# Kernel optimization log

Measured on AMD Instinct MI355X. Metric: run time of the kernel, lower is better.

## Reference

```python
import jax, jax.numpy as jnp
import numpy as np

L, I, D, N, K = 2, 8192, 2048, 2048, 32


def setup_inputs() -> dict:
    key = jax.random.key(0)
    k1, k2, k3, k4 = jax.random.split(key, 4)
    gate = jax.random.normal(k1, (L, I, D), dtype=jnp.float32) * (1.0 / np.sqrt(D).astype(np.float32))
    up = jax.random.normal(k2, (L, I, D), dtype=jnp.float32) * (1.0 / np.sqrt(D).astype(np.float32))
    down = jax.random.normal(k3, (L, D, I), dtype=jnp.float32) * (1.0 / np.sqrt(I).astype(np.float32))
    x = jax.random.normal(k4, (N, D), dtype=jnp.float32)
    return {"x": x, "gate": gate, "up": up, "down": down, "layer_idx": 0, "top_k": K}


def reference(x, gate, up, down, layer_idx, top_k):
    # Select frozen per-layer MLP weights
    g_w = gate[layer_idx]   # [I, D]
    u_w = up[layer_idx]     # [I, D]
    d_w = down[layer_idx]   # [D, I]
    # Full gate activations (needed to pick top-k neurons)
    g_full = jax.nn.silu(x @ g_w.T)                    # [N, I]
    # Top-k neurons per token by |gate activation|
    _, idx = jax.lax.top_k(jnp.abs(g_full), top_k)     # [N, K] int32
    g_sel = jnp.take_along_axis(g_full, idx, axis=-1)  # [N, K]
    # Gather-dot up projection: only the selected neuron rows
    u_sel = jnp.einsum('nkd,nd->nk', u_w[idx], x)      # [N, K]
    gu = g_sel * u_sel                                 # [N, K]
    # Gather-weighted-sum down projection: down.T rows for selected neurons
    out = jnp.einsum('nk,nkd->nd', gu, jnp.swapaxes(d_w, 0, 1)[idx])  # [N, D]
    return out
```

## Files before the change

kernel.cpp:

```cpp
#include <hip/hip_runtime.h>
#include <hip/hip_fp16.h>
#include <math.h>

constexpr int LI = 8192;
constexpr int LD = 2048;
constexpr int LN = 2048;
constexpr int LK = 32;
constexpr int CAP = 192;
constexpr int DEPTH = 96;

typedef short short8 __attribute__((ext_vector_type(8)));
typedef unsigned short ushort8 __attribute__((ext_vector_type(8)));
typedef _Float16 half8 __attribute__((ext_vector_type(8)));
typedef float f32x4 __attribute__((ext_vector_type(4)));
typedef const __attribute__((address_space(1))) void* gas1_t;
typedef __attribute__((address_space(3))) void* las3_t;

__device__ __forceinline__ void gload16(const void* g, void* l) {
    __builtin_amdgcn_global_load_lds((gas1_t)g, (las3_t)l, 16, 0, 0);
}
__device__ __forceinline__ unsigned short f2bf_rne(float f) {
    unsigned u = __float_as_uint(f);
    return (unsigned short)((u + 0x7fffu + ((u >> 16) & 1u)) >> 16);
}
__device__ __forceinline__ unsigned short f2h_rne(float f) {
    return __half_as_ushort(__float2half(f));
}
__device__ __forceinline__ float h2f(unsigned short u) {
    return __half2float(__ushort_as_half(u));
}

__global__ __launch_bounds__(256) void k_cvt2(
    const float* __restrict__ x, const float* __restrict__ gate,
    const int* __restrict__ layer_idx,
    unsigned short* __restrict__ xh, unsigned short* __restrict__ wh,
    int* __restrict__ ghist)
{
    if (blockIdx.x >= 2560) {
        int t = threadIdx.x;
        #pragma unroll
        for (int b = 0; b < 32; ++b) ghist[t * 32 + b] = 0;
        return;
    }
    const float* src; unsigned short* dst; int n8, bid, nb;
    if (blockIdx.x < 512) {
        src = x; dst = xh; n8 = (LN * LD) / 8; bid = blockIdx.x; nb = 512;
    } else {
        src = gate + (size_t)layer_idx[0] * LI * LD; dst = wh;
        n8 = (LI * LD) / 8; bid = blockIdx.x - 512; nb = 2048;
    }
    int i = bid * 256 + threadIdx.x;
    int stride = nb * 256;
    for (; i < n8; i += stride) {
        f32x4 v0 = *(const f32x4*)(src + 8 * (size_t)i);
        f32x4 v1 = *(const f32x4*)(src + 8 * (size_t)i + 4);
        ushort8 h;
        h[0] = f2h_rne(v0[0]); h[1] = f2h_rne(v0[1]);
        h[2] = f2h_rne(v0[2]); h[3] = f2h_rne(v0[3]);
        h[4] = f2h_rne(v1[0]); h[5] = f2h_rne(v1[1]);
        h[6] = f2h_rne(v1[2]); h[7] = f2h_rne(v1[3]);
        ((ushort8*)dst)[i] = h;
    }
}

__global__ __launch_bounds__(256) void k_gemmT(
    const unsigned short* __restrict__ xh, const unsigned short* __restrict__ wh,
    const float* __restrict__ down, const int* __restrict__ layer_idx,
    unsigned short* __restrict__ zk, unsigned short* __restrict__ dTb)
{
    __shared__ char smem[32768];
    const int tid = threadIdx.x;

    if (blockIdx.x >= 1024) {
        float (*t)[65] = (float(*)[65])smem;
        const float* __restrict__ dw = down + (size_t)layer_idx[0] * LD * LI;
        const int bid2 = blockIdx.x - 1024;
        const int bi = (bid2 & 127) * 64;
        const int bd = (bid2 >> 7) * 64;
        const int tx = tid & 63, ty = tid >> 6;
        #pragma unroll
        for (int it = 0; it < 16; ++it) {
            int r = ty + it * 4;
            t[r][tx] = dw[(size_t)(bd + r) * LI + bi + tx];
        }
        __syncthreads();
        #pragma unroll
        for (int it = 0; it < 16; ++it) {
            int rr = ty + it * 4;
            dTb[(size_t)(bi + rr) * LD + bd + tx] = f2bf_rne(t[tx][rr]);
        }
        return;
    }

    short* Ah = (short*)smem;
    short* Bh = (short*)smem + 8192;

    const int w = tid >> 6, lane = tid & 63;
    const int flat = blockIdx.x;
    const int xcd  = flat & 7;
    const int l    = flat >> 3;
    const int bi = (xcd * 8 + (l & 7)) * 128;
    const int bn = (l >> 3) * 128;

    const int srow   = w * 32 + (lane >> 3);
    const int schunk = (lane & 7) ^ ((lane >> 3) & 7);
    const unsigned short* xbh = xh + (size_t)(bn + srow) * LD + schunk * 8;
    const unsigned short* wbh = wh + (size_t)(bi + srow) * LD + schunk * 8;

    f32x4 acc[4][4];
    #pragma unroll
    for (int m = 0; m < 4; ++m)
        #pragma unroll
        for (int n = 0; n < 4; ++n) acc[m][n] = (f32x4){0.f, 0.f, 0.f, 0.f};

    const int wm = (w >> 1) * 64, wn = (w & 1) * 64;

    #define STAGE(k0)                                                          \
        {                                                                      \
            _Pragma("unroll")                                                  \
            for (int t = 0; t < 4; ++t) {                                      \
                int ldo = (w * 32 + t * 8) * 64;                               \
                size_t go = (size_t)t * 8 * LD + (k0);                         \
                gload16(xbh + go, Ah + ldo);                                   \
                gload16(wbh + go, Bh + ldo);                                   \
            }                                                                  \
        }

    STAGE(0);
    __syncthreads();
    for (int k0 = 0;;) {
        #pragma unroll
        for (int ks = 0; ks < 2; ++ks) {
            half8 a_h[4], b_h[4];
            #pragma unroll
            for (int m = 0; m < 4; ++m) {
                int lr = wm + m * 16 + (lane & 15);
                int lc = ks * 4 + (lane >> 4);
                a_h[m] = *(const half8*)(Ah + lr * 64 + ((lc ^ (lr & 7)) << 3));
            }
            #pragma unroll
            for (int n = 0; n < 4; ++n) {
                int lr = wn + n * 16 + (lane & 15);
                int lc = ks * 4 + (lane >> 4);
                b_h[n] = *(const half8*)(Bh + lr * 64 + ((lc ^ (lr & 7)) << 3));
            }
            #pragma unroll
            for (int m = 0; m < 4; ++m)
                #pragma unroll
                for (int n = 0; n < 4; ++n)
                    acc[m][n] = __builtin_amdgcn_mfma_f32_16x16x32_f16(a_h[m], b_h[n], acc[m][n], 0, 0, 0);
        }
        k0 += 64;
        if (k0 >= LD) break;
        __syncthreads();
        STAGE(k0);
        __syncthreads();
    }

    #pragma unroll
    for (int m = 0; m < 4; ++m) {
        int rb = bn + wm + m * 16 + (lane >> 4) * 4;
        #pragma unroll
        for (int n = 0; n < 4; ++n) {
            int cb = bi + wn + n * 16 + (lane & 15);
            #pragma unroll
            for (int r = 0; r < 4; ++r) {
                float zv = acc[m][n][r];
                float g = zv / (1.f + expf(-zv));
                zk[(size_t)(rb + r) * LI + cb] = f2h_rne(fabsf(g));
            }
        }
    }
    #undef STAGE
}

__global__ __launch_bounds__(256) void k_select(
    const unsigned short* __restrict__ zk, int* __restrict__ band,
    int* __restrict__ bandcnt, int* __restrict__ ghist, int* __restrict__ inv)
{
    __shared__ int hist[2048];
    __shared__ int sums[256];
    __shared__ int base_s;
    __shared__ int thrbin_s;

    const int row = blockIdx.x;
    const int tid = threadIdx.x;
    const int lane = tid & 63;
    const unsigned short* __restrict__ z = zk + (size_t)row * LI;

    if (tid == 0) { thrbin_s = 0; base_s = 0; }
    for (int i = tid; i < 2048; i += 256) hist[i] = 0;
    __syncthreads();

    ushort8 kv[4];
    #pragma unroll
    for (int c = 0; c < 4; ++c) {
        kv[c] = *(const ushort8*)(z + c * 2048 + tid * 8);
        #pragma unroll
        for (int j = 0; j < 8; ++j) {
            int b = (int)(kv[c][j] >> 2) - 3328;
            if (b > 0) {
                b = b > 2047 ? 2047 : b;
                atomicAdd(&hist[b], 1);
            }
        }
    }
    __syncthreads();

    int own = 0;
    #pragma unroll
    for (int b = 0; b < 8; ++b) own += hist[tid * 8 + b];
    sums[tid] = own;
    __syncthreads();
    for (int st = 1; st < 256; st <<= 1) {
        int v = (tid + st < 256) ? sums[tid + st] : 0;
        __syncthreads();
        sums[tid] += v;
        __syncthreads();
    }
    int after = (tid < 255) ? sums[tid + 1] : 0;
    if (after < LK && after + own >= LK) {
        int cum = after;
        for (int b = 7; b >= 0; --b) {
            cum += hist[tid * 8 + b];
            if (cum >= LK) { thrbin_s = tid * 8 + b; break; }
        }
    }
    __syncthreads();
    const float bandlo =
        h2f((unsigned short)((thrbin_s + 3328) << 2)) - 0.012f;

    #pragma unroll
    for (int c = 0; c < 4; ++c) {
        unsigned flags = 0;
        #pragma unroll
        for (int j = 0; j < 8; ++j) {
            if (h2f(kv[c][j]) >= bandlo) flags |= (1u << j);
        }
        int cnt = __popc(flags);
        int pre = cnt;
        #pragma unroll
        for (int o = 1; o < 64; o <<= 1) {
            int v = __shfl_up(pre, o);
            if (lane >= o) pre += v;
        }
        int wtotal = __shfl(pre, 63);
        int excl = pre - cnt;
        int wbase = 0;
        if (lane == 63 && wtotal) wbase = atomicAdd(&base_s, wtotal);
        wbase = __shfl(wbase, 63);
        int pos = wbase + excl;
        while (flags) {
            int j = __ffs(flags) - 1;
            flags &= flags - 1;
            if (pos < CAP) {
                int gi = c * 2048 + tid * 8 + j;
                band[row * CAP + pos] = gi;
                int p = atomicAdd(&ghist[gi], 1);
                if (p < DEPTH) inv[gi * DEPTH + p] = (row << 8) | pos;
            }
            ++pos;
        }
    }
    __syncthreads();
    if (tid == 0) bandcnt[row] = base_s < CAP ? base_s : CAP;
}

__global__ __launch_bounds__(256) void k_pair(
    const float* __restrict__ x, const float* __restrict__ gate,
    const float* __restrict__ up, const int* __restrict__ layer_idx,
    const int* __restrict__ ghist, const int* __restrict__ inv,
    float* __restrict__ gdot, float* __restrict__ udot)
{
    __shared__ float gs[LD];
    __shared__ float us[LD];
    const int j = blockIdx.x;
    const int tid = threadIdx.x;
    const int lane = tid & 63, w = tid >> 6;
    int nj = ghist[j];
    if (nj == 0) return;
    if (nj > DEPTH) nj = DEPTH;
    const float* __restrict__ gr = gate + (size_t)layer_idx[0] * LI * LD + (size_t)j * LD;
    const float* __restrict__ ur = up   + (size_t)layer_idx[0] * LI * LD + (size_t)j * LD;
    for (int i = tid * 4; i < LD; i += 1024) {
        *(f32x4*)&gs[i] = *(const f32x4*)(gr + i);
        *(f32x4*)&us[i] = *(const f32x4*)(ur + i);
    }
    __syncthreads();
    const int base = j * DEPTH;
    for (int e = w; e < nj; e += 4) {
        int packed = inv[base + e];
        int row = packed >> 8, slot = packed & 255;
        const float* __restrict__ xr = x + (size_t)row * LD;
        float gd0 = 0.f, gd1 = 0.f, ud0 = 0.f, ud1 = 0.f;
        #pragma unroll
        for (int it = 0; it < 8; it += 2) {
            int i0 = lane * 4 + it * 256;
            int i1 = i0 + 256;
            f32x4 xa = *(const f32x4*)(xr + i0);
            f32x4 xb = *(const f32x4*)(xr + i1);
            gd0 = fmaf(xa[0], gs[i0+0], gd0); gd0 = fmaf(xa[1], gs[i0+1], gd0);
            gd0 = fmaf(xa[2], gs[i0+2], gd0); gd0 = fmaf(xa[3], gs[i0+3], gd0);
            ud0 = fmaf(xa[0], us[i0+0], ud0); ud0 = fmaf(xa[1], us[i0+1], ud0);
            ud0 = fmaf(xa[2], us[i0+2], ud0); ud0 = fmaf(xa[3], us[i0+3], ud0);
            gd1 = fmaf(xb[0], gs[i1+0], gd1); gd1 = fmaf(xb[1], gs[i1+1], gd1);
            gd1 = fmaf(xb[2], gs[i1+2], gd1); gd1 = fmaf(xb[3], gs[i1+3], gd1);
            ud1 = fmaf(xb[0], us[i1+0], ud1); ud1 = fmaf(xb[1], us[i1+1], ud1);
            ud1 = fmaf(xb[2], us[i1+2], ud1); ud1 = fmaf(xb[3], us[i1+3], ud1);
        }
        float gd = gd0 + gd1, ud = ud0 + ud1;
        #pragma unroll
        for (int o = 32; o; o >>= 1) {
            gd += __shfl_down(gd, o);
            ud += __shfl_down(ud, o);
        }
        if (lane == 0) {
            gdot[(size_t)row * CAP + slot] = gd;
            udot[(size_t)row * CAP + slot] = ud;
        }
    }
}

__global__ __launch_bounds__(256) void k_finaldown(
    const int* __restrict__ band, const int* __restrict__ bandcnt,
    const float* __restrict__ gdot, const float* __restrict__ udot,
    const unsigned short* __restrict__ dTb, float* __restrict__ out)
{
    __shared__ float ckey[CAP];
    __shared__ float cgu[CAP];
    __shared__ int   cidx[CAP];
    __shared__ int   js[LK];
    __shared__ float wgt[LK];
    const int row = blockIdx.x;
    const int tid = threadIdx.x;
    const int lane = tid & 63;
    const int cnt = bandcnt[row];
    if (tid < CAP) { ckey[tid] = -1.f; cgu[tid] = 0.f; cidx[tid] = 0x7fffffff; }
    __syncthreads();
    if (tid < cnt) {
        float gd = gdot[(size_t)row * CAP + tid];
        float g = gd / (1.f + expf(-gd));
        ckey[tid] = fabsf(g);
        cgu[tid]  = g * udot[(size_t)row * CAP + tid];
        cidx[tid] = band[row * CAP + tid];
    }
    __syncthreads();
    if (tid < 64) {
        float k1 = ckey[lane], k2 = ckey[lane + 64], k3 = ckey[lane + 128];
        int   i1 = cidx[lane], i2 = cidx[lane + 64], i3 = cidx[lane + 128];
        int   p1 = lane, p2 = lane + 64, p3 = lane + 128;
        for (int slot = 0; slot < LK; ++slot) {
            float bk = k1; int bi_ = i1, bp = p1;
            if (k2 > bk || (k2 == bk && i2 < bi_)) { bk = k2; bi_ = i2; bp = p2; }
            if (k3 > bk || (k3 == bk && i3 < bi_)) { bk = k3; bi_ = i3; bp = p3; }
            #pragma unroll
            for (int o = 1; o < 64; o <<= 1) {
                float ok = __shfl_xor(bk, o);
                int  oi = __shfl_xor(bi_, o);
                int  op = __shfl_xor(bp, o);
                if (ok > bk || (ok == bk && oi < bi_)) { bk = ok; bi_ = oi; bp = op; }
            }
            if (lane == 0) {
                js[slot]  = bi_ & (LI - 1);
                wgt[slot] = cgu[bp < CAP ? bp : 0];
            }
            if (p1 == bp) { k1 = -1.f; i1 = 0x7fffffff; }
            if (p2 == bp) { k2 = -1.f; i2 = 0x7fffffff; }
            if (p3 == bp) { k3 = -1.f; i3 = 0x7fffffff; }
        }
    }
    __syncthreads();

    float a[8] = {0.f,0.f,0.f,0.f,0.f,0.f,0.f,0.f};
    #pragma unroll 4
    for (int k = 0; k < LK; ++k) {
        const ushort8 v = *(const ushort8*)(dTb + (size_t)js[k] * LD + tid * 8);
        float wv = wgt[k];
        #pragma unroll
        for (int e = 0; e < 8; ++e)
            a[e] = fmaf(wv, __uint_as_float(((unsigned)v[e]) << 16), a[e]);
    }
    float* o = out + (size_t)row * LD + tid * 8;
    f32x4 o0 = {a[0], a[1], a[2], a[3]};
    f32x4 o1 = {a[4], a[5], a[6], a[7]};
    *(f32x4*)o = o0;
    *(f32x4*)(o + 4) = o1;
}

extern "C" void kernel_launch(void* const* d_in, const int* in_sizes, int n_in,
                              void* d_out, int out_size, void* d_ws, size_t ws_size,
                              hipStream_t stream)
{
    const float* x      = (const float*)d_in[0];
    const float* gate   = (const float*)d_in[1];
    const float* up     = (const float*)d_in[2];
    const float* down   = (const float*)d_in[3];
    const int* layer_idx = (const int*)d_in[4];
    float* out = (float*)d_out;

    const size_t NC_ = (size_t)LN * CAP;
    char* p = (char*)d_ws;
    int*   band    = (int*)p;            p += NC_ * 4;
    int*   bandcnt = (int*)p;            p += (size_t)LN * 4;
    int*   ghist   = (int*)p;            p += (size_t)LI * 4;
    int*   inv     = (int*)p;            p += (size_t)LI * DEPTH * 4;
    float* gdot    = (float*)p;          p += NC_ * 4;
    float* udot    = (float*)p;          p += NC_ * 4;
    p = (char*)(((size_t)p + 255) & ~(size_t)255);

    const size_t xcnt = (size_t)LN * LD;
    const size_t wcnt = (size_t)LI * LD;
    unsigned short* xh = (unsigned short*)p;
    unsigned short* wh = xh + xcnt;
    unsigned short* zk = wh + wcnt;
    unsigned short* dTb = zk + (size_t)LN * LI;
    char* big_end = (char*)(dTb + (size_t)LI * LD);

    if ((size_t)(big_end - (char*)d_ws) > ws_size) return;

    k_cvt2<<<2561, 256, 0, stream>>>(x, gate, layer_idx, xh, wh, ghist);
    k_gemmT<<<5120, 256, 0, stream>>>(xh, wh, down, layer_idx, zk, dTb);
    k_select<<<LN, 256, 0, stream>>>(zk, band, bandcnt, ghist, inv);
    k_pair<<<LI, 256, 0, stream>>>(x, gate, up, layer_idx, ghist, inv, gdot, udot);
    k_finaldown<<<LN, 256, 0, stream>>>(band, bandcnt, gdot, udot, dTb, out);
}
```

Measured before the change: 270.5 us.

## Skip exact gate recompute for candidates clearly above the top-k threshold

The GEMM now stores the signed fp16 SiLU gate value, and selection splits candidates into sure-in ones and boundary ones using a second, higher threshold. Only boundary candidates get the exact fp32 gate dot product in k_pair. Sure candidates reuse the fp16 gate and compute the up dot from fp16 x. Gate rows are loaded only for neurons that have boundary entries. This cuts fp32 gate row traffic and FMA work, but the output now uses fp16-approximated gate and x values for most selected neurons, which lowers accuracy.

Result: faster. 244.9 us (-9.5%).

```diff
diff --git a/kernel.cpp b/kernel.cpp
--- a/kernel.cpp
+++ b/kernel.cpp
@@ -34,12 +34,15 @@
     const float* __restrict__ x, const float* __restrict__ gate,
     const int* __restrict__ layer_idx,
     unsigned short* __restrict__ xh, unsigned short* __restrict__ wh,
-    int* __restrict__ ghist)
+    int* __restrict__ ghist, int* __restrict__ gbnd)
 {
     if (blockIdx.x >= 2560) {
         int t = threadIdx.x;
         #pragma unroll
-        for (int b = 0; b < 32; ++b) ghist[t * 32 + b] = 0;
+        for (int b = 0; b < 32; ++b) {
+            ghist[t * 32 + b] = 0;
+            gbnd[t * 32 + b]  = 0;
+        }
         return;
     }
     const float* src; unsigned short* dst; int n8, bid, nb;
@@ -167,7 +170,7 @@
             for (int r = 0; r < 4; ++r) {
                 float zv = acc[m][n][r];
                 float g = zv / (1.f + expf(-zv));
-                zk[(size_t)(rb + r) * LI + cb] = f2h_rne(fabsf(g));
+                zk[(size_t)(rb + r) * LI + cb] = f2h_rne(g);
             }
         }
     }
@@ -176,7 +179,8 @@
 
 __global__ __launch_bounds__(256) void k_select(
     const unsigned short* __restrict__ zk, int* __restrict__ band,
-    int* __restrict__ bandcnt, int* __restrict__ ghist, int* __restrict__ inv)
+    int* __restrict__ bandcnt, int* __restrict__ ghist,
+    int* __restrict__ gbnd, int* __restrict__ inv)
 {
     __shared__ int hist[2048];
     __shared__ int sums[256];
@@ -198,7 +202,8 @@
         kv[c] = *(const ushort8*)(z + c * 2048 + tid * 8);
         #pragma unroll
         for (int j = 0; j < 8; ++j) {
-            int b = (int)(kv[c][j] >> 2) - 3328;
+            int ka = (int)(kv[c][j] & 0x7FFF);
+            int b = (ka >> 2) - 3328;
             if (b > 0) {
                 b = b > 2047 ? 2047 : b;
                 atomicAdd(&hist[b], 1);
@@ -229,13 +234,19 @@
     __syncthreads();
     const float bandlo =
         h2f((unsigned short)((thrbin_s + 3328) << 2)) - 0.012f;
+    const float thr_sure =
+        h2f((unsigned short)((thrbin_s + 1 + 3328) << 2)) + 0.024f;
 
     #pragma unroll
     for (int c = 0; c < 4; ++c) {
-        unsigned flags = 0;
+        unsigned flags = 0, bflags = 0;
         #pragma unroll
         for (int j = 0; j < 8; ++j) {
-            if (h2f(kv[c][j]) >= bandlo) flags |= (1u << j);
+            float kf = h2f((unsigned short)(kv[c][j] & 0x7FFF));
+            if (kf >= bandlo) {
+                flags |= (1u << j);
+                if (kf < thr_sure) bflags |= (1u << j);
+            }
         }
         int cnt = __popc(flags);
         int pre = cnt;
@@ -253,11 +264,13 @@
         while (flags) {
             int j = __ffs(flags) - 1;
             flags &= flags - 1;
+            int bnd = (bflags >> j) & 1;
             if (pos < CAP) {
                 int gi = c * 2048 + tid * 8 + j;
-                band[row * CAP + pos] = gi;
+                band[row * CAP + pos] = gi | (bnd << 15);
                 int p = atomicAdd(&ghist[gi], 1);
-                if (p < DEPTH) inv[gi * DEPTH + p] = (row << 8) | pos;
+                if (p < DEPTH) inv[gi * DEPTH + p] = (row << 9) | (bnd << 8) | pos;
+                if (bnd) atomicAdd(&gbnd[gi], 1);
             }
             ++pos;
         }
@@ -267,9 +280,11 @@
 }
 
 __global__ __launch_bounds__(256) void k_pair(
-    const float* __restrict__ x, const float* __restrict__ gate,
-    const float* __restrict__ up, const int* __restrict__ layer_idx,
-    const int* __restrict__ ghist, const int* __restrict__ inv,
+    const float* __restrict__ x, const unsigned short* __restrict__ xh,
+    const float* __restrict__ gate, const float* __restrict__ up,
+    const int* __restrict__ layer_idx,
+    const int* __restrict__ ghist, const int* __restrict__ gbnd,
+    const int* __restrict__ inv,
     float* __restrict__ gdot, float* __restrict__ udot)
 {
     __shared__ float gs[LD];
@@ -280,43 +295,68 @@
     int nj = ghist[j];
     if (nj == 0) return;
     if (nj > DEPTH) nj = DEPTH;
-    const float* __restrict__ gr = gate + (size_t)layer_idx[0] * LI * LD + (size_t)j * LD;
-    const float* __restrict__ ur = up   + (size_t)layer_idx[0] * LI * LD + (size_t)j * LD;
-    for (int i = tid * 4; i < LD; i += 1024) {
-        *(f32x4*)&gs[i] = *(const f32x4*)(gr + i);
+    const int hasb = gbnd[j];
+    const float* __restrict__ ur = up + (size_t)layer_idx[0] * LI * LD + (size_t)j * LD;
+    for (int i = tid * 4; i < LD; i += 1024)
         *(f32x4*)&us[i] = *(const f32x4*)(ur + i);
+    if (hasb) {
+        const float* __restrict__ gr = gate + (size_t)layer_idx[0] * LI * LD + (size_t)j * LD;
+        for (int i = tid * 4; i < LD; i += 1024)
+            *(f32x4*)&gs[i] = *(const f32x4*)(gr + i);
     }
     __syncthreads();
     const int base = j * DEPTH;
     for (int e = w; e < nj; e += 4) {
         int packed = inv[base + e];
-        int row = packed >> 8, slot = packed & 255;
-        const float* __restrict__ xr = x + (size_t)row * LD;
-        float gd0 = 0.f, gd1 = 0.f, ud0 = 0.f, ud1 = 0.f;
-        #pragma unroll
-        for (int it = 0; it < 8; it += 2) {
-            int i0 = lane * 4 + it * 256;
-            int i1 = i0 + 256;
-            f32x4 xa = *(const f32x4*)(xr + i0);
-            f32x4 xb = *(const f32x4*)(xr + i1);
-            gd0 = fmaf(xa[0], gs[i0+0], gd0); gd0 = fmaf(xa[1], gs[i0+1], gd0);
-            gd0 = fmaf(xa[2], gs[i0+2], gd0); gd0 = fmaf(xa[3], gs[i0+3], gd0);
-            ud0 = fmaf(xa[0], us[i0+0], ud0); ud0 = fmaf(xa[1], us[i0+1], ud0);
-            ud0 = fmaf(xa[2], us[i0+2], ud0); ud0 = fmaf(xa[3], us[i0+3], ud0);
-            gd1 = fmaf(xb[0], gs[i1+0], gd1); gd1 = fmaf(xb[1], gs[i1+1], gd1);
-            gd1 = fmaf(xb[2], gs[i1+2], gd1); gd1 = fmaf(xb[3], gs[i1+3], gd1);
-            ud1 = fmaf(xb[0], us[i1+0], ud1); ud1 = fmaf(xb[1], us[i1+1], ud1);
-            ud1 = fmaf(xb[2], us[i1+2], ud1); ud1 = fmaf(xb[3], us[i1+3], ud1);
-        }
-        float gd = gd0 + gd1, ud = ud0 + ud1;
-        #pragma unroll
-        for (int o = 32; o; o >>= 1) {
-            gd += __shfl_down(gd, o);
-            ud += __shfl_down(ud, o);
-        }
-        if (lane == 0) {
-            gdot[(size_t)row * CAP + slot] = gd;
-            udot[(size_t)row * CAP + slot] = ud;
+        int row = packed >> 9, bnd = (packed >> 8) & 1, slot = packed & 255;
+        if (bnd) {
+            const float* __restrict__ xr = x + (size_t)row * LD;
+            float gd0 = 0.f, gd1 = 0.f, ud0 = 0.f, ud1 = 0.f;
+            #pragma unroll
+            for (int it = 0; it < 8; it += 2) {
+                int i0 = lane * 4 + it * 256;
+                int i1 = i0 + 256;
+                f32x4 xa = *(const f32x4*)(xr + i0);
+                f32x4 xb = *(const f32x4*)(xr + i1);
+                gd0 = fmaf(xa[0], gs[i0+0], gd0); gd0 = fmaf(xa[1], gs[i0+1], gd0);
+                gd0 = fmaf(xa[2], gs[i0+2], gd0); gd0 = fmaf(xa[3], gs[i0+3], gd0);
+                ud0 = fmaf(xa[0], us[i0+0], ud0); ud0 = fmaf(xa[1], us[i0+1], ud0);
+                ud0 = fmaf(xa[2], us[i0+2], ud0); ud0 = fmaf(xa[3], us[i0+3], ud0);
+                gd1 = fmaf(xb[0], gs[i1+0], gd1); gd1 = fmaf(xb[1], gs[i1+1], gd1);
+                gd1 = fmaf(xb[2], gs[i1+2], gd1); gd1 = fmaf(xb[3], gs[i1+3], gd1);
+                ud1 = fmaf(xb[0], us[i1+0], ud1); ud1 = fmaf(xb[1], us[i1+1], ud1);
+                ud1 = fmaf(xb[2], us[i1+2], ud1); ud1 = fmaf(xb[3], us[i1+3], ud1);
+            }
+            float gd = gd0 + gd1, ud = ud0 + ud1;
+            #pragma unroll
+            for (int o = 32; o; o >>= 1) {
+                gd += __shfl_down(gd, o);
+                ud += __shfl_down(ud, o);
+            }
+            if (lane == 0) {
+                gdot[(size_t)row * CAP + slot] = gd;
+                udot[(size_t)row * CAP + slot] = ud;
+            }
+        } else {
+            const unsigned short* __restrict__ xrh = xh + (size_t)row * LD;
+            float ud0 = 0.f, ud1 = 0.f;
+            #pragma unroll
+            for (int it = 0; it < 4; ++it) {
+                int ib = lane * 8 + it * 512;
+                ushort8 hv = *(const ushort8*)(xrh + ib);
+                ud0 = fmaf(h2f(hv[0]), us[ib+0], ud0);
+                ud0 = fmaf(h2f(hv[1]), us[ib+1], ud0);
+                ud0 = fmaf(h2f(hv[2]), us[ib+2], ud0);
+                ud0 = fmaf(h2f(hv[3]), us[ib+3], ud0);
+                ud1 = fmaf(h2f(hv[4]), us[ib+4], ud1);
+                ud1 = fmaf(h2f(hv[5]), us[ib+5], ud1);
+                ud1 = fmaf(h2f(hv[6]), us[ib+6], ud1);
+                ud1 = fmaf(h2f(hv[7]), us[ib+7], ud1);
+            }
+            float ud = ud0 + ud1;
+            #pragma unroll
+            for (int o = 32; o; o >>= 1) ud += __shfl_down(ud, o);
+            if (lane == 0) udot[(size_t)row * CAP + slot] = ud;
         }
     }
 }
@@ -324,6 +364,7 @@
 __global__ __launch_bounds__(256) void k_finaldown(
     const int* __restrict__ band, const int* __restrict__ bandcnt,
     const float* __restrict__ gdot, const float* __restrict__ udot,
+    const unsigned short* __restrict__ zk,
     const unsigned short* __restrict__ dTb, float* __restrict__ out)
 {
     __shared__ float ckey[CAP];
@@ -338,11 +379,19 @@
     if (tid < CAP) { ckey[tid] = -1.f; cgu[tid] = 0.f; cidx[tid] = 0x7fffffff; }
     __syncthreads();
     if (tid < cnt) {
-        float gd = gdot[(size_t)row * CAP + tid];
-        float g = gd / (1.f + expf(-gd));
-        ckey[tid] = fabsf(g);
+        int v = band[row * CAP + tid];
+        int gi = v & (LI - 1);
+        float g;
+        if ((v >> 15) & 1) {
+            float gd = gdot[(size_t)row * CAP + tid];
+            g = gd / (1.f + expf(-gd));
+            ckey[tid] = fabsf(g);
+        } else {
+            g = h2f(zk[(size_t)row * LI + gi]);
+            ckey[tid] = 1e30f;
+        }
         cgu[tid]  = g * udot[(size_t)row * CAP + tid];
-        cidx[tid] = band[row * CAP + tid];
+        cidx[tid] = gi;
     }
     __syncthreads();
     if (tid < 64) {
@@ -403,6 +452,7 @@
     int*   band    = (int*)p;            p += NC_ * 4;
     int*   bandcnt = (int*)p;            p += (size_t)LN * 4;
     int*   ghist   = (int*)p;            p += (size_t)LI * 4;
+    int*   gbnd    = (int*)p;            p += (size_t)LI * 4;
     int*   inv     = (int*)p;            p += (size_t)LI * DEPTH * 4;
     float* gdot    = (float*)p;          p += NC_ * 4;
     float* udot    = (float*)p;          p += NC_ * 4;
@@ -418,9 +468,10 @@
 
     if ((size_t)(big_end - (char*)d_ws) > ws_size) return;
 
-    k_cvt2<<<2561, 256, 0, stream>>>(x, gate, layer_idx, xh, wh, ghist);
+    k_cvt2<<<2561, 256, 0, stream>>>(x, gate, layer_idx, xh, wh, ghist, gbnd);
     k_gemmT<<<5120, 256, 0, stream>>>(xh, wh, down, layer_idx, zk, dTb);
-    k_select<<<LN, 256, 0, stream>>>(zk, band, bandcnt, ghist, inv);
-    k_pair<<<LI, 256, 0, stream>>>(x, gate, up, layer_idx, ghist, inv, gdot, udot);
-    k_finaldown<<<LN, 256, 0, stream>>>(band, bandcnt, gdot, udot, dTb, out);
-}
+    k_select<<<LN, 256, 0, stream>>>(zk, band, bandcnt, ghist, gbnd, inv);
+    k_pair<<<LI, 256, 0, stream>>>(x, xh, gate, up, layer_idx, ghist, gbnd, inv,
+                                   gdot, udot);
+    k_finaldown<<<LN, 256, 0, stream>>>(band, bandcnt, gdot, udot, zk, dTb, out);
+}
```
